# Optimization experiments

Hardware: AMD Instinct MI355X
Metric: run time of the kernel (lower is better)

Reference implementation:

```python
import jax, jax.numpy as jnp
import numpy as np

B, T, D = 128, 1024, 128

def setup_inputs() -> dict:
    key = jax.random.key(0)
    k1, k2 = jax.random.split(key)
    x = jax.random.normal(k1, (B, T, 3 * D), dtype=jnp.float32)
    # original init: kernel = gain * eye(d_dim); use eye plus small noise for a nontrivial test
    kernel = jnp.eye(D, dtype=jnp.float32) + 0.01 * jax.random.normal(k2, (D, D), dtype=jnp.float32)
    return {"x": x, "kernel": kernel}

def reference(x, kernel):
    d = kernel.shape[0]
    # x: (B, T, 3d) -> channel blocks (module permutes to (B,C,T) then back; net effect is slicing last dim)
    y = x[:, :, :d]            # (B, T, d) observed values
    w = x[:, :, d:2 * d]       # (B, T, d) log-intensities
    y_obs = x[:, :, 2 * d:3 * d]  # (B, T, d) transient targets
    intensity = jnp.exp(w)
    # softmax across channels per timestep (exp(w - logsumexp_d w))
    sm = jax.nn.softmax(w, axis=2)
    mean = jnp.mean(y, axis=1, keepdims=True)  # (B, 1, d), broadcast over T
    # cross-channel mixing: small per-timestep d x d matmul
    smooth = jnp.matmul(sm * (y - mean), kernel) + mean  # (B, T, d)
    y_trans = y_obs - smooth
    # concat order matches torch.cat([rep1, intensity, y_trans], dim=1) after final permute
    return jnp.concatenate([smooth, intensity, y_trans], axis=-1)  # (B, T, 3d)
```

## Files before the change

### kernel.cpp

```cpp
#include <hip/hip_runtime.h>
#include <cstdint>

#define D_CH 128
#define T_LEN 1024
#define ROWLEN 384
#define NROWS (128 * 1024)
#define TILE 64
#define NCHUNK (NROWS / TILE)
#define VSTR_B 272
#define EPI_W 132
#define SLICE_B 8448

typedef __attribute__((ext_vector_type(8))) _Float16 f16x8;
typedef __attribute__((ext_vector_type(4))) _Float16 f16x4;
typedef __attribute__((ext_vector_type(4))) float f32x4;

__global__ __launch_bounds__(1024) void prep_kernel(const float* __restrict__ x,
                                                    const float* __restrict__ Kmat,
                                                    float* __restrict__ meang,
                                                    _Float16* __restrict__ Ktg,
                                                    int S, int JITER) {
  int bid = blockIdx.x;
  int bh = bid / S;
  int tq = bid - bh * S;
  int b = bh >> 1, h = bh & 1;
  int tid = threadIdx.x;
  int li = tid & 15, tt = tid >> 4;
  int d4 = h * 64 + 4 * li;
  f32x4 s = {0.f, 0.f, 0.f, 0.f};
  const float* xp = x + (size_t)b * T_LEN * ROWLEN + d4;
  int t0 = tq * (T_LEN / S) + tt;
#pragma unroll 4
  for (int j = 0; j < JITER; ++j) {
    int t = t0 + 64 * j;
    f32x4 v = *(const f32x4*)(xp + (size_t)t * ROWLEN);
    s += v;
  }
  __shared__ f32x4 red[64][17];
  red[tt][li] = s;
  __syncthreads();
  for (int st = 32; st > 0; st >>= 1) {
    if (tt < st) red[tt][li] += red[tt + st][li];
    __syncthreads();
  }
  if (tt == 0) {
    f32x4 m = red[0][li] * (1.0f / 1024.0f);
    *(f32x4*)(meang + (size_t)(b * S + tq) * D_CH + d4) = m;
  }
  if (tq == 0 && tid < 64) {
    int f = bh * 64 + tid;
    int j = f & 7;
    int lane = (f >> 3) & 63;
    int q = f >> 9;
    int ks = q & 3, nt = q >> 2;
    int kk = ks * 32 + (lane >> 4) * 8 + j;
    int nn = nt * 16 + (lane & 15);
    Ktg[f] = (_Float16)Kmat[kk * D_CH + nn];
  }
}

__global__ __launch_bounds__(256, 4) void main_kernel(const float* __restrict__ x,
                                                      const float* __restrict__ meang,
                                                      const _Float16* __restrict__ Ktg,
                                                      float* __restrict__ out,
                                                      int S) {
  __shared__ alignas(16) char smem[4 * SLICE_B];
  int tid = threadIdx.x;
  int wave = tid >> 6, lane = tid & 63;
  int hf = lane >> 5, li = lane & 31;
  int c0 = 4 * li;
  int m0 = wave * 16;
  int l15 = lane & 15, lg = lane >> 4;
  char* vslice = smem + wave * SLICE_B;
  float* epi = (float*)(smem + wave * SLICE_B);
  int chunk = blockIdx.x;
  int row0 = chunk * TILE;
  int bb = chunk >> 4;
  f32x4 mn = {0.f, 0.f, 0.f, 0.f};
  for (int s = 0; s < S; ++s)
    mn += *(const f32x4*)(meang + (size_t)(bb * S + s) * D_CH + c0);

  f32x4 yb[8], wb[8];
#pragma unroll
  for (int i = 0; i < 8; ++i) {
    size_t base = (size_t)(row0 + m0 + 2 * i + hf) * ROWLEN + c0;
    yb[i] = __builtin_nontemporal_load((const f32x4*)(x + base));
    wb[i] = __builtin_nontemporal_load((const f32x4*)(x + base + 128));
  }
#pragma unroll
  for (int i = 0; i < 8; ++i) {
    int lr = 2 * i + hf;
    int row = row0 + m0 + lr;
    f32x4 e;
    e[0] = __expf(wb[i][0]); e[1] = __expf(wb[i][1]);
    e[2] = __expf(wb[i][2]); e[3] = __expf(wb[i][3]);
    __builtin_nontemporal_store(e, (f32x4*)(out + (size_t)row * ROWLEN + 128 + c0));
    float s = e[0] + e[1] + e[2] + e[3];
    s += __shfl_xor(s, 1, 32);
    s += __shfl_xor(s, 2, 32);
    s += __shfl_xor(s, 4, 32);
    s += __shfl_xor(s, 8, 32);
    s += __shfl_xor(s, 16, 32);
    float rinv = 1.0f / s;
    f16x4 vh;
    vh[0] = (_Float16)(e[0] * rinv * (yb[i][0] - mn[0]));
    vh[1] = (_Float16)(e[1] * rinv * (yb[i][1] - mn[1]));
    vh[2] = (_Float16)(e[2] * rinv * (yb[i][2] - mn[2]));
    vh[3] = (_Float16)(e[3] * rinv * (yb[i][3] - mn[3]));
    *(f16x4*)(vslice + lr * VSTR_B + li * 8) = vh;
  }

  f32x4 yo[8];
#pragma unroll
  for (int i = 0; i < 8; ++i) {
    size_t base = (size_t)(row0 + m0 + 2 * i + hf) * ROWLEN + c0;
    yo[i] = __builtin_nontemporal_load((const f32x4*)(x + base + 256));
  }

  f16x8 a[4];
#pragma unroll
  for (int ks = 0; ks < 4; ++ks)
    a[ks] = *(const f16x8*)(vslice + l15 * VSTR_B + ks * 64 + lg * 16);
  f32x4 acc[8];
#pragma unroll
  for (int nt = 0; nt < 8; ++nt) {
    acc[nt] = (f32x4){0.f, 0.f, 0.f, 0.f};
#pragma unroll
    for (int ks = 0; ks < 4; ++ks) {
      f16x8 bf = *(const f16x8*)&Ktg[((nt * 4 + ks) * 64 + lane) * 8];
      acc[nt] = __builtin_amdgcn_mfma_f32_16x16x32_f16(a[ks], bf, acc[nt], 0, 0, 0);
    }
  }

#pragma unroll
  for (int nt = 0; nt < 8; ++nt)
#pragma unroll
    for (int r = 0; r < 4; ++r)
      epi[(lg * 4 + r) * EPI_W + nt * 16 + l15] = acc[nt][r];

#pragma unroll
  for (int i = 0; i < 8; ++i) {
    int lr = 2 * i + hf;
    size_t ob = (size_t)(row0 + m0 + lr) * ROWLEN;
    f32x4 sm4 = *(const f32x4*)&epi[lr * EPI_W + c0];
    sm4 += mn;
    __builtin_nontemporal_store(sm4, (f32x4*)(out + ob + c0));
    f32x4 yt = yo[i] - sm4;
    __builtin_nontemporal_store(yt, (f32x4*)(out + ob + 256 + c0));
  }
}

extern "C" void kernel_launch(void* const* d_in, const int* in_sizes, int n_in,
                              void* d_out, int out_size, void* d_ws, size_t ws_size,
                              hipStream_t stream) {
  const float* x = (const float*)d_in[0];
  const float* Kmat = (const float*)d_in[1];
  float* out = (float*)d_out;
  int S = (ws_size >= (size_t)(2 * 65536 + 32768)) ? 2 : 1;
  float* meang = (float*)d_ws;
  _Float16* Ktg = (_Float16*)((char*)d_ws + (size_t)S * 65536);
  prep_kernel<<<256 * S, 1024, 0, stream>>>(x, Kmat, meang, Ktg, S, 16 / S);
  main_kernel<<<NCHUNK, 256, 0, stream>>>(x, meang, Ktg, out, S);
}
```

Measured before the change: 336.5 us.

## Fuse mean reduction and main pass into one cooperative grid-synced kernel

Replaces the separate mean-reduction pre-pass with a single cooperative kernel. Each block loads its y and w rows once, writes the intensities, keeps the softmax-weighted fp16 operands in registers and publishes per-block partial sums of y. It then grid-syncs and applies the mean correction by folding -mean*K into a second MFMA. This removes the extra full read of the y channels and one kernel launch. In exchange it adds a grid-wide barrier, doubles the MFMA work, and quantises the mean to fp16 inside the matmul, which can cost accuracy. If the cooperative launch fails, it falls back to the old two-kernel path.

```diff
diff --git a/kernel.cpp b/kernel.cpp
--- a/kernel.cpp
+++ b/kernel.cpp
@@ -1,5 +1,8 @@
 #include <hip/hip_runtime.h>
+#include <hip/hip_cooperative_groups.h>
 #include <cstdint>
+
+namespace cg = cooperative_groups;
 
 #define D_CH 128
 #define T_LEN 1024
@@ -9,11 +12,169 @@
 #define NCHUNK (NROWS / TILE)
 #define VSTR_B 272
 #define EPI_W 132
-#define SLICE_B 8448
+#define WSLICE 8704
+#define MEAN_OFF (4 * WSLICE)
+#define SMEM_B (MEAN_OFF + 512)
 
 typedef __attribute__((ext_vector_type(8))) _Float16 f16x8;
 typedef __attribute__((ext_vector_type(4))) _Float16 f16x4;
 typedef __attribute__((ext_vector_type(4))) float f32x4;
+
+__global__ __launch_bounds__(256, 4) void fused_kernel(const float* __restrict__ x,
+                                                       const float* __restrict__ Kmat,
+                                                       float* __restrict__ part,
+                                                       _Float16* __restrict__ Ktg,
+                                                       float* __restrict__ out) {
+  __shared__ alignas(16) char smem[SMEM_B];
+  cg::grid_group grid = cg::this_grid();
+  int bid = blockIdx.x;
+  int tid = threadIdx.x;
+  int wave = tid >> 6, lane = tid & 63;
+  int hf = lane >> 5, li = lane & 31;
+  int c0 = 4 * li;
+  int m0 = wave * 16;
+  int l15 = lane & 15, lg = lane >> 4;
+  char* vs1 = smem + wave * WSLICE;
+  char* vs2 = vs1 + 4352;
+  float* epi = (float*)(smem + wave * WSLICE);
+  float* mean_lds = (float*)(smem + MEAN_OFF);
+  int b = bid >> 3;
+
+  if (bid < 256 && tid < 64) {
+    int f = bid * 64 + tid;
+    int j = f & 7;
+    int ln = (f >> 3) & 63;
+    int q = f >> 9;
+    int ks = q & 3, nt = q >> 2;
+    int kk = ks * 32 + (ln >> 4) * 8 + j;
+    int nn = nt * 16 + (ln & 15);
+    Ktg[f] = (_Float16)Kmat[kk * D_CH + nn];
+  }
+
+  f16x8 a1[2][4], a2[2][4];
+  f32x4 psum = {0.f, 0.f, 0.f, 0.f};
+#pragma unroll
+  for (int c = 0; c < 2; ++c) {
+    int row0 = (2 * bid + c) * TILE;
+    f32x4 yb[8], wb[8];
+#pragma unroll
+    for (int i = 0; i < 8; ++i) {
+      size_t base = (size_t)(row0 + m0 + 2 * i + hf) * ROWLEN + c0;
+      yb[i] = __builtin_nontemporal_load((const f32x4*)(x + base));
+      wb[i] = __builtin_nontemporal_load((const f32x4*)(x + base + 128));
+    }
+#pragma unroll
+    for (int i = 0; i < 8; ++i) {
+      int lr = 2 * i + hf;
+      int row = row0 + m0 + lr;
+      psum += yb[i];
+      f32x4 e;
+      e[0] = __expf(wb[i][0]); e[1] = __expf(wb[i][1]);
+      e[2] = __expf(wb[i][2]); e[3] = __expf(wb[i][3]);
+      __builtin_nontemporal_store(e, (f32x4*)(out + (size_t)row * ROWLEN + 128 + c0));
+      float s = e[0] + e[1] + e[2] + e[3];
+      s += __shfl_xor(s, 1, 32);
+      s += __shfl_xor(s, 2, 32);
+      s += __shfl_xor(s, 4, 32);
+      s += __shfl_xor(s, 8, 32);
+      s += __shfl_xor(s, 16, 32);
+      float rinv = 1.0f / s;
+      f16x4 v1, v2;
+      v1[0] = (_Float16)(e[0] * rinv * yb[i][0]);
+      v1[1] = (_Float16)(e[1] * rinv * yb[i][1]);
+      v1[2] = (_Float16)(e[2] * rinv * yb[i][2]);
+      v1[3] = (_Float16)(e[3] * rinv * yb[i][3]);
+      v2[0] = (_Float16)(e[0] * rinv);
+      v2[1] = (_Float16)(e[1] * rinv);
+      v2[2] = (_Float16)(e[2] * rinv);
+      v2[3] = (_Float16)(e[3] * rinv);
+      *(f16x4*)(vs1 + lr * VSTR_B + li * 8) = v1;
+      *(f16x4*)(vs2 + lr * VSTR_B + li * 8) = v2;
+    }
+#pragma unroll
+    for (int ks = 0; ks < 4; ++ks) {
+      a1[c][ks] = *(const f16x8*)(vs1 + l15 * VSTR_B + ks * 64 + lg * 16);
+      a2[c][ks] = *(const f16x8*)(vs2 + l15 * VSTR_B + ks * 64 + lg * 16);
+    }
+  }
+
+  __syncthreads();
+  f32x4* scratch = (f32x4*)smem;
+  scratch[(wave * 2 + hf) * 32 + li] = psum;
+  __syncthreads();
+  if (tid < 32) {
+    f32x4 t = scratch[tid];
+#pragma unroll
+    for (int k = 1; k < 8; ++k) t += scratch[k * 32 + tid];
+    *(f32x4*)(part + (size_t)bid * D_CH + 4 * tid) = t;
+  }
+  __threadfence();
+  grid.sync();
+  __threadfence();
+
+  if (tid < 32) {
+    f32x4 t = {0.f, 0.f, 0.f, 0.f};
+#pragma unroll
+    for (int k = 0; k < 8; ++k)
+      t += *(const f32x4*)(part + (size_t)(b * 8 + k) * D_CH + 4 * tid);
+    t *= (1.0f / 1024.0f);
+    *(f32x4*)(mean_lds + 4 * tid) = t;
+  }
+  __syncthreads();
+
+  f16x8 nm[4];
+#pragma unroll
+  for (int ks = 0; ks < 4; ++ks) {
+    f32x4 lo = *(const f32x4*)(mean_lds + ks * 32 + lg * 8);
+    f32x4 hi = *(const f32x4*)(mean_lds + ks * 32 + lg * 8 + 4);
+    f16x8 m;
+    m[0] = (_Float16)(-lo[0]); m[1] = (_Float16)(-lo[1]);
+    m[2] = (_Float16)(-lo[2]); m[3] = (_Float16)(-lo[3]);
+    m[4] = (_Float16)(-hi[0]); m[5] = (_Float16)(-hi[1]);
+    m[6] = (_Float16)(-hi[2]); m[7] = (_Float16)(-hi[3]);
+    nm[ks] = m;
+  }
+
+#pragma unroll
+  for (int c = 0; c < 2; ++c) {
+    int row0 = (2 * bid + c) * TILE;
+    f32x4 acc[8];
+#pragma unroll
+    for (int nt = 0; nt < 8; ++nt) {
+      acc[nt] = (f32x4){0.f, 0.f, 0.f, 0.f};
+#pragma unroll
+      for (int ks = 0; ks < 4; ++ks) {
+        f16x8 bf = *(const f16x8*)&Ktg[((nt * 4 + ks) * 64 + lane) * 8];
+        acc[nt] = __builtin_amdgcn_mfma_f32_16x16x32_f16(a1[c][ks], bf, acc[nt], 0, 0, 0);
+        f16x8 b2 = bf * nm[ks];
+        acc[nt] = __builtin_amdgcn_mfma_f32_16x16x32_f16(a2[c][ks], b2, acc[nt], 0, 0, 0);
+      }
+    }
+#pragma unroll
+    for (int nt = 0; nt < 8; ++nt)
+#pragma unroll
+      for (int r = 0; r < 4; ++r)
+        epi[(lg * 4 + r) * EPI_W + nt * 16 + l15] = acc[nt][r];
+
+    f32x4 yo[8];
+#pragma unroll
+    for (int i = 0; i < 8; ++i) {
+      size_t base = (size_t)(row0 + m0 + 2 * i + hf) * ROWLEN + c0;
+      yo[i] = __builtin_nontemporal_load((const f32x4*)(x + base + 256));
+    }
+    f32x4 mn = *(const f32x4*)(mean_lds + c0);
+#pragma unroll
+    for (int i = 0; i < 8; ++i) {
+      int lr = 2 * i + hf;
+      size_t ob = (size_t)(row0 + m0 + lr) * ROWLEN;
+      f32x4 sm4 = *(const f32x4*)&epi[lr * EPI_W + c0];
+      sm4 += mn;
+      __builtin_nontemporal_store(sm4, (f32x4*)(out + ob + c0));
+      f32x4 yt = yo[i] - sm4;
+      __builtin_nontemporal_store(yt, (f32x4*)(out + ob + 256 + c0));
+    }
+  }
+}
 
 __global__ __launch_bounds__(1024) void prep_kernel(const float* __restrict__ x,
                                                     const float* __restrict__ Kmat,
@@ -50,11 +211,11 @@
   if (tq == 0 && tid < 64) {
     int f = bh * 64 + tid;
     int j = f & 7;
-    int lane = (f >> 3) & 63;
+    int ln = (f >> 3) & 63;
     int q = f >> 9;
     int ks = q & 3, nt = q >> 2;
-    int kk = ks * 32 + (lane >> 4) * 8 + j;
-    int nn = nt * 16 + (lane & 15);
+    int kk = ks * 32 + (ln >> 4) * 8 + j;
+    int nn = nt * 16 + (ln & 15);
     Ktg[f] = (_Float16)Kmat[kk * D_CH + nn];
   }
 }
@@ -64,15 +225,15 @@
                                                       const _Float16* __restrict__ Ktg,
                                                       float* __restrict__ out,
                                                       int S) {
-  __shared__ alignas(16) char smem[4 * SLICE_B];
+  __shared__ alignas(16) char smem[4 * 8448];
   int tid = threadIdx.x;
   int wave = tid >> 6, lane = tid & 63;
   int hf = lane >> 5, li = lane & 31;
   int c0 = 4 * li;
   int m0 = wave * 16;
   int l15 = lane & 15, lg = lane >> 4;
-  char* vslice = smem + wave * SLICE_B;
-  float* epi = (float*)(smem + wave * SLICE_B);
+  char* vslice = smem + wave * 8448;
+  float* epi = (float*)(smem + wave * 8448);
   int chunk = blockIdx.x;
   int row0 = chunk * TILE;
   int bb = chunk >> 4;
@@ -109,14 +270,12 @@
     vh[3] = (_Float16)(e[3] * rinv * (yb[i][3] - mn[3]));
     *(f16x4*)(vslice + lr * VSTR_B + li * 8) = vh;
   }
-
   f32x4 yo[8];
 #pragma unroll
   for (int i = 0; i < 8; ++i) {
     size_t base = (size_t)(row0 + m0 + 2 * i + hf) * ROWLEN + c0;
     yo[i] = __builtin_nontemporal_load((const f32x4*)(x + base + 256));
   }
-
   f16x8 a[4];
 #pragma unroll
   for (int ks = 0; ks < 4; ++ks)
@@ -131,13 +290,11 @@
       acc[nt] = __builtin_amdgcn_mfma_f32_16x16x32_f16(a[ks], bf, acc[nt], 0, 0, 0);
     }
   }
-
 #pragma unroll
   for (int nt = 0; nt < 8; ++nt)
 #pragma unroll
     for (int r = 0; r < 4; ++r)
       epi[(lg * 4 + r) * EPI_W + nt * 16 + l15] = acc[nt][r];
-
 #pragma unroll
   for (int i = 0; i < 8; ++i) {
     int lr = 2 * i + hf;
@@ -156,6 +313,16 @@
   const float* x = (const float*)d_in[0];
   const float* Kmat = (const float*)d_in[1];
   float* out = (float*)d_out;
+
+  if (ws_size >= (size_t)(512 * 1024 + 32 * 1024)) {
+    float* part = (float*)d_ws;
+    _Float16* Ktg = (_Float16*)((char*)d_ws + 512 * 1024);
+    void* args[] = {(void*)&x, (void*)&Kmat, (void*)&part, (void*)&Ktg, (void*)&out};
+    hipError_t e = hipLaunchCooperativeKernel((const void*)fused_kernel, dim3(1024),
+                                              dim3(256), args, 0, stream);
+    if (e == hipSuccess) return;
+  }
+
   int S = (ws_size >= (size_t)(2 * 65536 + 32768)) ? 2 : 1;
   float* meang = (float*)d_ws;
   _Float16* Ktg = (_Float16*)((char*)d_ws + (size_t)S * 65536);
```

After: 714.6 us. +112.4%, slower.
